# Kernel tuning notes

Hardware: AMD Instinct MI355X
Metric: run time of the kernel (lower is better)

## Reference

```python
import jax, jax.numpy as jnp
import numpy as np


def _bilinear(x, oh, ow, align_corners):
    # x: [N, C, H, W] -> [N, C, oh, ow], matching torch bilinear semantics
    n, c, h, w = x.shape
    if align_corners:
        ys = jnp.linspace(0.0, h - 1.0, oh)
        xs = jnp.linspace(0.0, w - 1.0, ow)
    else:
        ys = jnp.clip((jnp.arange(oh) + 0.5) * (h / oh) - 0.5, 0.0, h - 1.0)
        xs = jnp.clip((jnp.arange(ow) + 0.5) * (w / ow) - 0.5, 0.0, w - 1.0)
    y0 = jnp.floor(ys).astype(jnp.int32)
    y1 = jnp.minimum(y0 + 1, h - 1)
    x0 = jnp.floor(xs).astype(jnp.int32)
    x1 = jnp.minimum(x0 + 1, w - 1)
    wy = (ys - y0).astype(x.dtype)[None, None, :, None]
    wx = (xs - x0).astype(x.dtype)[None, None, None, :]
    rows = x[:, :, y0, :] * (1.0 - wy) + x[:, :, y1, :] * wy  # [N,C,oh,W]
    out = rows[:, :, :, x0] * (1.0 - wx) + rows[:, :, :, x1] * wx  # [N,C,oh,ow]
    return out


def _minmax_norm(m):
    # per-sample min-max normalize over (C,H,W)
    mn = m.min(axis=(1, 2, 3), keepdims=True)
    mx = m.max(axis=(1, 2, 3), keepdims=True)
    return (m - mn) / (mx - mn)


def setup_inputs() -> dict:
    key = jax.random.key(0)
    k1, k2, k3, k4, k5, k6 = jax.random.split(key, 6)
    B, C, H, W = 32, 256, 56, 56
    Ce, He, We = 128, 28, 28
    return {
        "main_inputs": jax.random.normal(k1, (B, C, H, W), dtype=jnp.float32),
        "embedding_inputs": jax.random.normal(k2, (B, Ce, He, We), dtype=jnp.float32),
        "inference_x": jax.random.uniform(k3, (B, 1, 112, 112), dtype=jnp.float32),
        "conv_w": jax.random.normal(k4, (C, Ce), dtype=jnp.float32) * 0.05,
        "conv_b": jax.random.normal(k5, (C,), dtype=jnp.float32) * 0.05,
        "weight": jax.random.normal(k6, (1,), dtype=jnp.float32),
    }


def reference(main_inputs, embedding_inputs, inference_x, conv_w, conv_b, weight):
    H, W = main_inputs.shape[2], main_inputs.shape[3]
    # interface: bilinear upsample (align_corners=False) + 1x1 conv
    emb = _bilinear(embedding_inputs, H, W, align_corners=False)
    emb = jnp.einsum('nchw,oc->nohw', emb, conv_w) + conv_b[None, :, None, None]
    # channel mean -> per-sample min-max normalize
    mask = _minmax_norm(emb.mean(axis=1, keepdims=True))  # [B,1,H,W]
    # inference mask: bilinear (align_corners=True) to mask resolution
    inf = _bilinear(inference_x, H, W, align_corners=True)
    mask = _minmax_norm(mask * inf)
    a = jax.nn.sigmoid(main_inputs)
    return a * mask * weight[0] + a
```

## Files before the change

### kernel.cpp

```cpp
#include <hip/hip_runtime.h>
#include <math.h>


#define HW_E 784
#define HW_O 3136
#define CE   128
#define CO   256
#define NB   32
#define KS   8
#define CPP  (CE / KS)
#define NPE  (NB * HW_E)

#define ERED_OFF 0
#define S_OFF    (KS * NPE)

typedef float f4 __attribute__((ext_vector_type(4)));

__global__ __launch_bounds__(256) void k_ered(const float* __restrict__ emb,
                                              const float* __restrict__ W,
                                              float* __restrict__ ered) {
    __shared__ float swp[4][CPP];
    __shared__ float swb[CPP];
    const int t   = threadIdx.x;
    const int gid = blockIdx.x * 256 + t;
    const int part = gid / NPE;
    const int cb   = part * CPP;

    {
        const int j  = t & 15;
        const int oc = t >> 4;
        const float* wp = W + (size_t)(oc * 16) * CE + cb + j;
        float a = 0.f;
        #pragma unroll
        for (int k = 0; k < 16; ++k) a += wp[(size_t)k * CE];
        a += __shfl_xor(a, 16, 64);
        a += __shfl_xor(a, 32, 64);
        if ((t & 63) < CPP) swp[t >> 6][j] = a;
    }
    __syncthreads();
    if (t < CPP) swb[t] = swp[0][t] + swp[1][t] + swp[2][t] + swp[3][t];
    __syncthreads();

    const int local = gid - part * NPE;
    const int n = local / HW_E;
    const int p = local - n * HW_E;
    const float* base = emb + ((size_t)n * CE + cb) * HW_E + p;
    float acc = 0.f;
    #pragma unroll
    for (int c = 0; c < CPP; ++c) acc += base[(size_t)c * HW_E] * swb[c];
    ered[gid] = acc;
}

__device__ inline void bmm(float lmin, float lmax, float* red, int t,
                           float& mn, float& mx) {
    __syncthreads();
    #pragma unroll
    for (int off = 32; off; off >>= 1) {
        lmin = fminf(lmin, __shfl_down(lmin, off, 64));
        lmax = fmaxf(lmax, __shfl_down(lmax, off, 64));
    }
    if ((t & 63) == 0) { red[t >> 6] = lmin; red[16 + (t >> 6)] = lmax; }
    __syncthreads();
    if (t == 0) {
        float a = red[0], b = red[16];
        #pragma unroll
        for (int i = 1; i < 16; ++i) { a = fminf(a, red[i]); b = fmaxf(b, red[16 + i]); }
        red[0] = a; red[16] = b;
    }
    __syncthreads();
    mn = red[0]; mx = red[16];
}

__global__ __launch_bounds__(1024) void k_mask(const float* __restrict__ infx,
                                               const float* __restrict__ ered,
                                               const float* __restrict__ wscalar,
                                               float* __restrict__ sout) {
    __shared__ float sE[HW_E];
    __shared__ float sM[HW_O];
    __shared__ float red[32];
    const int n = blockIdx.x;
    const int t = threadIdx.x;

    if (t < HW_E) {
        float v = 0.f;
        #pragma unroll
        for (int k = 0; k < KS; ++k) v += ered[k * NPE + n * HW_E + t];
        sE[t] = v;
    }
    __syncthreads();

    float lmin = 1e30f, lmax = -1e30f;
    for (int p = t; p < HW_O; p += 1024) {
        int oh = p / 56, ow = p % 56;
        float ys = fminf(fmaxf(0.5f * oh - 0.25f, 0.f), 27.f);
        float xs = fminf(fmaxf(0.5f * ow - 0.25f, 0.f), 27.f);
        int y0 = (int)ys, x0 = (int)xs;
        int y1 = min(y0 + 1, 27), x1 = min(x0 + 1, 27);
        float wy = ys - (float)y0, wx = xs - (float)x0;
        float v00 = sE[y0 * 28 + x0], v01 = sE[y0 * 28 + x1];
        float v10 = sE[y1 * 28 + x0], v11 = sE[y1 * 28 + x1];
        float r0 = v00 * (1.f - wy) + v10 * wy;
        float r1 = v01 * (1.f - wy) + v11 * wy;
        float m  = r0 * (1.f - wx) + r1 * wx;
        sM[p] = m;
        lmin = fminf(lmin, m); lmax = fmaxf(lmax, m);
    }
    float mn1, mx1;
    bmm(lmin, lmax, red, t, mn1, mx1);
    float inv1 = 1.f / (mx1 - mn1);

    const float step = 111.0f / 55.0f;
    const float* xin = infx + (size_t)n * 112 * 112;
    float lmin2 = 1e30f, lmax2 = -1e30f;
    for (int p = t; p < HW_O; p += 1024) {
        int oh = p / 56, ow = p % 56;
        float ys = step * (float)oh, xs = step * (float)ow;
        int y0 = (int)ys, x0 = (int)xs;
        int y1 = min(y0 + 1, 111), x1 = min(x0 + 1, 111);
        float wy = ys - (float)y0, wx = xs - (float)x0;
        float v00 = xin[y0 * 112 + x0], v01 = xin[y0 * 112 + x1];
        float v10 = xin[y1 * 112 + x0], v11 = xin[y1 * 112 + x1];
        float r0 = v00 * (1.f - wy) + v10 * wy;
        float r1 = v01 * (1.f - wy) + v11 * wy;
        float inf = r0 * (1.f - wx) + r1 * wx;
        float p2 = (sM[p] - mn1) * inv1 * inf;
        sM[p] = p2;
        lmin2 = fminf(lmin2, p2); lmax2 = fmaxf(lmax2, p2);
    }
    float mn2, mx2;
    bmm(lmin2, lmax2, red, t, mn2, mx2);
    float inv2 = 1.f / (mx2 - mn2);
    float wgt = wscalar[0];

    for (int p = t; p < HW_O; p += 1024)
        sout[n * HW_O + p] = (sM[p] - mn2) * inv2 * wgt + 1.0f;
}

__global__ __launch_bounds__(256) void k_main(const float* __restrict__ x,
                                              const float* __restrict__ s,
                                              float* __restrict__ out, int total4) {
    const f4* x4 = (const f4*)x;
    const f4* s4 = (const f4*)s;
    f4* o4 = (f4*)out;
    const int q0 = blockIdx.x * 1024 + threadIdx.x;

    int q[4] = { q0, q0 + 256, q0 + 512, q0 + 768 };
    f4 v[4], sv[4];
    #pragma unroll
    for (int j = 0; j < 4; ++j)
        if (q[j] < total4) v[j] = __builtin_nontemporal_load(&x4[q[j]]);
    #pragma unroll
    for (int j = 0; j < 4; ++j)
        if (q[j] < total4) {
            int hwq = q[j] % (HW_O / 4);
            int n   = q[j] / ((HW_O / 4) * CO);
            sv[j] = s4[n * (HW_O / 4) + hwq];
        }
    #pragma unroll
    for (int j = 0; j < 4; ++j)
        if (q[j] < total4) {
            f4 r;
            r.x = sv[j].x / (1.f + expf(-v[j].x));
            r.y = sv[j].y / (1.f + expf(-v[j].y));
            r.z = sv[j].z / (1.f + expf(-v[j].z));
            r.w = sv[j].w / (1.f + expf(-v[j].w));
            __builtin_nontemporal_store(r, &o4[q[j]]);
        }
}

extern "C" void kernel_launch(void* const* d_in, const int* in_sizes, int n_in,
                              void* d_out, int out_size, void* d_ws, size_t ws_size,
                              hipStream_t stream) {
    const float* main_in = (const float*)d_in[0];
    const float* emb_in  = (const float*)d_in[1];
    const float* inf_in  = (const float*)d_in[2];
    const float* conv_w  = (const float*)d_in[3];
    const float* weight  = (const float*)d_in[5];
    float* out = (float*)d_out;
    float* ws  = (float*)d_ws;

    k_ered<<<KS * NPE / 256, 256, 0, stream>>>(emb_in, conv_w, ws + ERED_OFF);
    k_mask<<<NB, 1024, 0, stream>>>(inf_in, ws + ERED_OFF, weight, ws + S_OFF);

    int total4 = out_size / 4;
    int blocks = (total4 + 1023) / 1024;
    k_main<<<blocks, 256, 0, stream>>>(main_in, ws + S_OFF, out, total4);
}
```

Baseline: 205.2 us.

## Fuse embedding channel reduction into mask kernel and use fast sigmoid intrinsics

Removes the separate k_ered kernel, which split the 128-channel weighted reduction across 8 partitions and staged partial sums in workspace. The mask kernel now sums the conv weights itself and reduces all 128 embedding channels per sample, which saves a launch and a workspace round trip. The cost is only 32 blocks, each with 784 active threads running a serial 128-channel loop, so far less parallelism for that phase. The main kernel also switches to hardware exp2 and rcp intrinsics for the sigmoid and gets an occupancy hint in its launch bounds.

```diff
diff --git a/kernel.cpp b/kernel.cpp
--- a/kernel.cpp
+++ b/kernel.cpp
@@ -7,49 +7,21 @@
 #define CE   128
 #define CO   256
 #define NB   32
-#define KS   8
-#define CPP  (CE / KS)
-#define NPE  (NB * HW_E)
-
-#define ERED_OFF 0
-#define S_OFF    (KS * NPE)
 
 typedef float f4 __attribute__((ext_vector_type(4)));
 
-__global__ __launch_bounds__(256) void k_ered(const float* __restrict__ emb,
-                                              const float* __restrict__ W,
-                                              float* __restrict__ ered) {
-    __shared__ float swp[4][CPP];
-    __shared__ float swb[CPP];
-    const int t   = threadIdx.x;
-    const int gid = blockIdx.x * 256 + t;
-    const int part = gid / NPE;
-    const int cb   = part * CPP;
-
-    {
-        const int j  = t & 15;
-        const int oc = t >> 4;
-        const float* wp = W + (size_t)(oc * 16) * CE + cb + j;
-        float a = 0.f;
-        #pragma unroll
-        for (int k = 0; k < 16; ++k) a += wp[(size_t)k * CE];
-        a += __shfl_xor(a, 16, 64);
-        a += __shfl_xor(a, 32, 64);
-        if ((t & 63) < CPP) swp[t >> 6][j] = a;
-    }
-    __syncthreads();
-    if (t < CPP) swb[t] = swp[0][t] + swp[1][t] + swp[2][t] + swp[3][t];
-    __syncthreads();
-
-    const int local = gid - part * NPE;
-    const int n = local / HW_E;
-    const int p = local - n * HW_E;
-    const float* base = emb + ((size_t)n * CE + cb) * HW_E + p;
-    float acc = 0.f;
-    #pragma unroll
-    for (int c = 0; c < CPP; ++c) acc += base[(size_t)c * HW_E] * swb[c];
-    ered[gid] = acc;
-}
+#if __has_builtin(__builtin_amdgcn_exp2f)
+__device__ inline float fexp2(float x) { return __builtin_amdgcn_exp2f(x); }
+#else
+__device__ inline float fexp2(float x) { return exp2f(x); }
+#endif
+#if __has_builtin(__builtin_amdgcn_rcpf)
+__device__ inline float frcp(float x) { return __builtin_amdgcn_rcpf(x); }
+#else
+__device__ inline float frcp(float x) { return 1.0f / x; }
+#endif
+#define LOG2E 1.4426950408889634f
+__device__ inline float fsig(float x) { return frcp(1.0f + fexp2(-LOG2E * x)); }
 
 __device__ inline void bmm(float lmin, float lmax, float* red, int t,
                            float& mn, float& mx) {
@@ -71,21 +43,43 @@
     mn = red[0]; mx = red[16];
 }
 
-__global__ __launch_bounds__(1024) void k_mask(const float* __restrict__ infx,
-                                               const float* __restrict__ ered,
-                                               const float* __restrict__ wscalar,
-                                               float* __restrict__ sout) {
+__global__ __launch_bounds__(1024) void k_premask(const float* __restrict__ emb,
+                                                  const float* __restrict__ W,
+                                                  const float* __restrict__ infx,
+                                                  const float* __restrict__ wscalar,
+                                                  float* __restrict__ sout) {
+    __shared__ float swp[8][CE];
+    __shared__ float swb[CE];
     __shared__ float sE[HW_E];
     __shared__ float sM[HW_O];
     __shared__ float red[32];
     const int n = blockIdx.x;
     const int t = threadIdx.x;
 
+    {
+        const int c  = t & 127;
+        const int og = t >> 7;
+        const float* wp = W + (size_t)(og * 32) * CE + c;
+        float a = 0.f;
+        #pragma unroll
+        for (int k = 0; k < 32; ++k) a += wp[(size_t)k * CE];
+        swp[og][c] = a;
+    }
+    __syncthreads();
+    if (t < CE) {
+        float a = 0.f;
+        #pragma unroll
+        for (int g = 0; g < 8; ++g) a += swp[g][t];
+        swb[t] = a;
+    }
+    __syncthreads();
+
     if (t < HW_E) {
-        float v = 0.f;
-        #pragma unroll
-        for (int k = 0; k < KS; ++k) v += ered[k * NPE + n * HW_E + t];
-        sE[t] = v;
+        const float* base = emb + (size_t)n * CE * HW_E + t;
+        float acc = 0.f;
+        #pragma unroll 8
+        for (int c = 0; c < CE; ++c) acc += base[(size_t)c * HW_E] * swb[c];
+        sE[t] = acc;
     }
     __syncthreads();
 
@@ -136,9 +130,9 @@
         sout[n * HW_O + p] = (sM[p] - mn2) * inv2 * wgt + 1.0f;
 }
 
-__global__ __launch_bounds__(256) void k_main(const float* __restrict__ x,
-                                              const float* __restrict__ s,
-                                              float* __restrict__ out, int total4) {
+__global__ __launch_bounds__(256, 8) void k_main(const float* __restrict__ x,
+                                                 const float* __restrict__ s,
+                                                 float* __restrict__ out, int total4) {
     const f4* x4 = (const f4*)x;
     const f4* s4 = (const f4*)s;
     f4* o4 = (f4*)out;
@@ -160,10 +154,10 @@
     for (int j = 0; j < 4; ++j)
         if (q[j] < total4) {
             f4 r;
-            r.x = sv[j].x / (1.f + expf(-v[j].x));
-            r.y = sv[j].y / (1.f + expf(-v[j].y));
-            r.z = sv[j].z / (1.f + expf(-v[j].z));
-            r.w = sv[j].w / (1.f + expf(-v[j].w));
+            r.x = sv[j].x * fsig(v[j].x);
+            r.y = sv[j].y * fsig(v[j].y);
+            r.z = sv[j].z * fsig(v[j].z);
+            r.w = sv[j].w * fsig(v[j].w);
             __builtin_nontemporal_store(r, &o4[q[j]]);
         }
 }
@@ -179,10 +173,9 @@
     float* out = (float*)d_out;
     float* ws  = (float*)d_ws;
 
-    k_ered<<<KS * NPE / 256, 256, 0, stream>>>(emb_in, conv_w, ws + ERED_OFF);
-    k_mask<<<NB, 1024, 0, stream>>>(inf_in, ws + ERED_OFF, weight, ws + S_OFF);
+    k_premask<<<NB, 1024, 0, stream>>>(emb_in, conv_w, inf_in, weight, ws);
 
     int total4 = out_size / 4;
     int blocks = (total4 + 1023) / 1024;
-    k_main<<<blocks, 256, 0, stream>>>(main_in, ws + S_OFF, out, total4);
+    k_main<<<blocks, 256, 0, stream>>>(main_in, ws, out, total4);
 }
```

Result: slower. 211.4 us (+3.0%).
